# Performance work log

Hardware: AMD Instinct MI355X
Metric: run time of the kernel (lower is better)

## Reference

```python
import jax, jax.numpy as jnp
import numpy as np

# --- Cone-beam geometry (TIGRE-style defaults) ---
B, C, A, V, U = 1, 8, 120, 128, 128   # batch, channels, angles, det_rows, det_cols
NZ, NY, NX = 96, 96, 96               # volume voxels (Z, Y, X)
DSO = 1000.0                          # source-to-origin distance (mm)
DSD = 1500.0                          # source-to-detector distance (mm)
DU = DV = 1.0                         # detector pixel size (mm)
DVOX = 0.8                            # voxel size (mm)


def setup_inputs() -> dict:
    key = jax.random.key(0)
    sinogram = jax.random.normal(key, (B, C, A, V, U), dtype=jnp.float32)
    angles = jnp.arange(A, dtype=jnp.float32) * jnp.float32(2.0 * np.pi / A)
    return {"sinogram": sinogram, "angles": angles}


def _voxel_grids():
    # Centered physical coordinates of the voxel grid (mm).
    z = (jnp.arange(NZ, dtype=jnp.float32) - (NZ - 1) / 2.0) * DVOX  # [NZ]
    y = (jnp.arange(NY, dtype=jnp.float32) - (NY - 1) / 2.0) * DVOX  # [NY]
    x = (jnp.arange(NX, dtype=jnp.float32) - (NX - 1) / 2.0) * DVOX  # [NX]
    return z[:, None, None], y[None, :, None], x[None, None, :]


def _backproject(sino_bc, angles):
    """Voxel-driven cone-beam backprojection (unfiltered, matched Atb style).

    sino_bc: [BC, A, V, U] -> volume [BC, NZ, NY, NX]
    """
    BC = sino_bc.shape[0]
    zg, yg, xg = _voxel_grids()
    nvox = NZ * NY * NX

    def step(acc, inp):
        ang, s_a = inp  # s_a: [BC, V, U]
        c, s = jnp.cos(ang), jnp.sin(ang)
        # Rotate voxel coords into the source frame for this angle.
        xr = xg * c + yg * s          # [1, NY, NX] distance along source axis
        yr = -xg * s + yg * c         # [1, NY, NX] lateral coordinate
        dist = DSO - xr               # source-to-voxel-plane distance
        mag = DSD / dist              # cone-beam magnification [1, NY, NX]
        iu = jnp.broadcast_to(yr * mag / DU + (U - 1) / 2.0, (NZ, NY, NX)).reshape(nvox)
        iv = (zg * mag / DV + (V - 1) / 2.0).reshape(nvox)
        w = jnp.broadcast_to(mag * mag, (NZ, NY, NX)).reshape(nvox)  # distance weight

        valid = (iu >= 0) & (iu <= U - 1) & (iv >= 0) & (iv <= V - 1)
        u0f = jnp.floor(iu); v0f = jnp.floor(iv)
        fu = iu - u0f; fv = iv - v0f
        u0 = jnp.clip(u0f.astype(jnp.int32), 0, U - 1)
        u1 = jnp.clip(u0 + 1, 0, U - 1)
        v0 = jnp.clip(v0f.astype(jnp.int32), 0, V - 1)
        v1 = jnp.clip(v0 + 1, 0, V - 1)

        # Bilinear detector interpolation for all channels at once: [BC, nvox]
        val = (s_a[:, v0, u0] * ((1 - fv) * (1 - fu))
               + s_a[:, v0, u1] * ((1 - fv) * fu)
               + s_a[:, v1, u0] * (fv * (1 - fu))
               + s_a[:, v1, u1] * (fv * fu))
        contrib = val * (w * valid.astype(jnp.float32))
        return acc + contrib, None

    acc0 = jnp.zeros((BC, nvox), dtype=jnp.float32)
    sino_a_first = jnp.moveaxis(sino_bc, 1, 0)  # [A, BC, V, U]
    acc, _ = jax.lax.scan(step, acc0, (angles, sino_a_first))
    return acc.reshape(BC, NZ, NY, NX)


def reference(sinogram, angles):
    b, c = sinogram.shape[:2]
    vol = _backproject(sinogram.reshape(b * c, A, V, U), angles)
    return vol.reshape(b, c, NZ, NY, NX)
```

## Files before the change

kernel.cpp:

```cpp
#include <hip/hip_runtime.h>
#include <hip/hip_fp16.h>


#define A_N   120
#define V_N   128
#define U_N   128
#define NZv   96
#define NYv   96
#define NXv   96
#define C_N   8
#define ZPT   2

constexpr float DSO  = 1000.0f;
constexpr float DSD  = 1500.0f;
constexpr float DVOX = 0.8f;

#define NVOX   (NZv * NYv * NXv)
#define SINO_N (A_N * V_N * U_N)
#define CHUNK  12

struct alignas(16) H8 { __half2 h[4]; };

__global__ __launch_bounds__(256) void sino_to_h(
    const float* __restrict__ in, H8* __restrict__ out) {
  int idx = blockIdx.x * 256 + threadIdx.x;
  H8 o;
#pragma unroll
  for (int i = 0; i < 4; ++i) {
    float lo = in[(size_t)(2 * i)     * SINO_N + idx];
    float hi = in[(size_t)(2 * i + 1) * SINO_N + idx];
    o.h[i] = __floats2half2_rn(lo, hi);
  }
  out[idx] = o;
}

__global__ __launch_bounds__(256) void backproject_t8(
    const H8* __restrict__ sino,
    const float* __restrict__ angles,
    float* __restrict__ out) {
  __shared__ float s_c[A_N];
  __shared__ float s_s[A_N];
  int tid = threadIdx.x;
  if (tid < A_N) {
    float a = angles[tid];
    s_c[tid] = cosf(a);
    s_s[tid] = sinf(a);
  }
  __syncthreads();

  int lid = tid & 63;
  int wv  = tid >> 6;
  int lx  = lid & 7;
  int ly  = lid >> 3;
  int x   = blockIdx.x * 16 + (wv & 1) * 8 + lx;
  int y   = blockIdx.y * 16 + (wv >> 1) * 8 + ly;
  int z0  = blockIdx.z * ZPT;

  float xf = ((float)x - (NXv - 1) * 0.5f) * DVOX;
  float yf = ((float)y - (NYv - 1) * 0.5f) * DVOX;
  float zf[ZPT];
#pragma unroll
  for (int k = 0; k < ZPT; ++k)
    zf[k] = ((float)(z0 + k) - (NZv - 1) * 0.5f) * DVOX;

  float2  accf[ZPT][4];
  __half2 acch[ZPT][4];
#pragma unroll
  for (int k = 0; k < ZPT; ++k)
#pragma unroll
    for (int i = 0; i < 4; ++i) {
      accf[k][i] = make_float2(0.0f, 0.0f);
      acch[k][i] = __float2half2_rn(0.0f);
    }

  for (int chnk = 0; chnk < A_N / CHUNK; ++chnk) {
#pragma unroll 2
    for (int j = 0; j < CHUNK; ++j) {
      int a = chnk * CHUNK + j;
      float cs = s_c[a], sn = s_s[a];
      float xr  = xf * cs + yf * sn;
      float yr  = yf * cs - xf * sn;
      float mag = DSD * __builtin_amdgcn_rcpf(DSO - xr);
      float w   = mag * mag;

      float iu  = yr * mag + (U_N - 1) * 0.5f;
      bool uok  = (iu >= 0.0f) && (iu <= (float)(U_N - 1));
      float iuc = fminf(fmaxf(iu, 0.0f), (float)(U_N - 1));
      float u0f = fminf(floorf(iuc), (float)(U_N - 2));
      float fu  = iuc - u0f;
      float gu  = 1.0f - fu;
      int u0    = (int)u0f;
      float wu  = uok ? w : 0.0f;
      const H8* arow = sino + (size_t)(a * (V_N * U_N) + u0);

#pragma unroll
      for (int k = 0; k < ZPT; ++k) {
        float iv  = fmaf(zf[k], mag, (V_N - 1) * 0.5f);
        bool ok   = (iv >= 0.0f) && (iv <= (float)(V_N - 1));
        float ivc = fminf(fmaxf(iv, 0.0f), (float)(V_N - 1));
        float v0f = fminf(floorf(ivc), (float)(V_N - 2));
        float fv  = ivc - v0f;
        int v0    = (int)v0f;
        float wz  = ok ? wu : 0.0f;
        float wv0 = wz * (1.0f - fv);
        float wv1 = wz * fv;

        __half2 h00 = __float2half2_rn(wv0 * gu);
        __half2 h01 = __float2half2_rn(wv0 * fu);
        __half2 h10 = __float2half2_rn(wv1 * gu);
        __half2 h11 = __float2half2_rn(wv1 * fu);

        const H8* p = arow + v0 * U_N;
        H8 c00 = p[0];
        H8 c01 = p[1];
        H8 c10 = p[U_N];
        H8 c11 = p[U_N + 1];

#pragma unroll
        for (int i = 0; i < 4; ++i) {
          acch[k][i] = __hfma2(c00.h[i], h00,
                       __hfma2(c01.h[i], h01,
                       __hfma2(c10.h[i], h10,
                       __hfma2(c11.h[i], h11, acch[k][i]))));
        }
      }
    }
#pragma unroll
    for (int k = 0; k < ZPT; ++k)
#pragma unroll
      for (int i = 0; i < 4; ++i) {
        float2 sf = __half22float2(acch[k][i]);
        accf[k][i].x += sf.x;
        accf[k][i].y += sf.y;
        acch[k][i] = __float2half2_rn(0.0f);
      }
  }

#pragma unroll
  for (int k = 0; k < ZPT; ++k) {
    int vi = ((z0 + k) * NYv + y) * NXv + x;
#pragma unroll
    for (int i = 0; i < 4; ++i) {
      out[(size_t)(2 * i)     * NVOX + vi] = accf[k][i].x;
      out[(size_t)(2 * i + 1) * NVOX + vi] = accf[k][i].y;
    }
  }
}

__global__ __launch_bounds__(256) void backproject_direct(
    const float* __restrict__ sino,
    const float* __restrict__ angles,
    float* __restrict__ out) {
  __shared__ float s_c[A_N];
  __shared__ float s_s[A_N];
  int tid = threadIdx.x;
  if (tid < A_N) {
    float a = angles[tid];
    s_c[tid] = cosf(a);
    s_s[tid] = sinf(a);
  }
  __syncthreads();

  int vi = blockIdx.x * 256 + tid;
  int x = vi % NXv;
  int t = vi / NXv;
  int y = t % NYv;
  int z = t / NYv;

  float xf = ((float)x - (NXv - 1) * 0.5f) * DVOX;
  float yf = ((float)y - (NYv - 1) * 0.5f) * DVOX;
  float zf = ((float)z - (NZv - 1) * 0.5f) * DVOX;

  float acc[C_N];
#pragma unroll
  for (int c = 0; c < C_N; ++c) acc[c] = 0.0f;

  for (int a = 0; a < A_N; ++a) {
    float cs = s_c[a], sn = s_s[a];
    float xr = xf * cs + yf * sn;
    float yr = yf * cs - xf * sn;
    float mag = DSD / (DSO - xr);
    float iu = yr * mag + (U_N - 1) * 0.5f;
    float iv = zf * mag + (V_N - 1) * 0.5f;
    if (iu < 0.0f || iu > (float)(U_N - 1) || iv < 0.0f || iv > (float)(V_N - 1))
      continue;
    float u0f = floorf(iu), v0f = floorf(iv);
    float fu = iu - u0f, fv = iv - v0f;
    int u0 = (int)u0f, v0 = (int)v0f;
    int u1 = min(u0 + 1, U_N - 1);
    int v1 = min(v0 + 1, V_N - 1);
    float w = mag * mag;
    float w00 = w * (1.0f - fv) * (1.0f - fu);
    float w01 = w * (1.0f - fv) * fu;
    float w10 = w * fv * (1.0f - fu);
    float w11 = w * fv * fu;

    int b00 = (a * V_N + v0) * U_N + u0;
    int b01 = (a * V_N + v0) * U_N + u1;
    int b10 = (a * V_N + v1) * U_N + u0;
    int b11 = (a * V_N + v1) * U_N + u1;
#pragma unroll
    for (int c = 0; c < C_N; ++c) {
      const float* pc = sino + (size_t)c * SINO_N;
      acc[c] += w00 * pc[b00] + w01 * pc[b01] + w10 * pc[b10] + w11 * pc[b11];
    }
  }

#pragma unroll
  for (int c = 0; c < C_N; ++c)
    out[(size_t)c * NVOX + vi] = acc[c];
}

extern "C" void kernel_launch(void* const* d_in, const int* in_sizes, int n_in,
                              void* d_out, int out_size, void* d_ws, size_t ws_size,
                              hipStream_t stream) {
  const float* sino   = (const float*)d_in[0];
  const float* angles = (const float*)d_in[1];
  float* out = (float*)d_out;

  size_t need = (size_t)SINO_N * sizeof(H8);
  if (ws_size >= need) {
    H8* sino_h = (H8*)d_ws;
    sino_to_h<<<SINO_N / 256, 256, 0, stream>>>(sino, sino_h);
    dim3 grid(NXv / 16, NYv / 16, NZv / ZPT);
    backproject_t8<<<grid, 256, 0, stream>>>(sino_h, angles, out);
  } else {
    backproject_direct<<<NVOX / 256, 256, 0, stream>>>(sino, angles, out);
  }
}
```

Measured before the change: 219.6 us.

## Stage per-angle detector footprint in LDS with double-buffered prefetch

For each block and angle, the kernel first computes a conservative 32x6 detector bounding box covering the block's 16x16x2 voxels. Each angle's patch of packed half-precision sinogram is loaded cooperatively into a double-buffered shared-memory array, and the next angle's patch is prefetched while the current one is used. Bilinear taps then read shared memory instead of doing scattered global gathers. In exchange it adds a block-wide barrier per angle and drops the inner-loop unroll. Samples that fall outside the fixed box are clamped, so correctness depends on the box always covering the true footprint.

```diff
diff --git a/kernel.cpp b/kernel.cpp
--- a/kernel.cpp
+++ b/kernel.cpp
@@ -10,6 +10,9 @@
 #define NXv   96
 #define C_N   8
 #define ZPT   2
+#define USPAN 32
+#define VSPAN 6
+#define NREC  (USPAN * VSPAN)
 
 constexpr float DSO  = 1000.0f;
 constexpr float DSD  = 1500.0f;
@@ -34,34 +37,63 @@
   out[idx] = o;
 }
 
-__global__ __launch_bounds__(256) void backproject_t8(
+__global__ __launch_bounds__(256) void backproject_lds(
     const H8* __restrict__ sino,
     const float* __restrict__ angles,
     float* __restrict__ out) {
   __shared__ float s_c[A_N];
   __shared__ float s_s[A_N];
+  __shared__ int2  s_box[A_N];
+  __shared__ H8    s_buf[2][NREC];
+
   int tid = threadIdx.x;
+  int bx0 = blockIdx.x * 16, by0 = blockIdx.y * 16;
+  int z0  = blockIdx.z * ZPT;
+  float zf0 = ((float)z0 - (NZv - 1) * 0.5f) * DVOX;
+  float zf1 = zf0 + DVOX;
+
   if (tid < A_N) {
-    float a = angles[tid];
-    s_c[tid] = cosf(a);
-    s_s[tid] = sinf(a);
+    float ang = angles[tid];
+    float cs = cosf(ang), sn = sinf(ang);
+    s_c[tid] = cs; s_s[tid] = sn;
+    float xl = ((float)bx0        - (NXv - 1) * 0.5f) * DVOX;
+    float xh = ((float)(bx0 + 15) - (NXv - 1) * 0.5f) * DVOX;
+    float yl = ((float)by0        - (NYv - 1) * 0.5f) * DVOX;
+    float yh = ((float)(by0 + 15) - (NYv - 1) * 0.5f) * DVOX;
+    float xrA = xl*cs + yl*sn, yrA = yl*cs - xl*sn;
+    float xrB = xl*cs + yh*sn, yrB = yh*cs - xl*sn;
+    float xrC = xh*cs + yl*sn, yrC = yl*cs - xh*sn;
+    float xrD = xh*cs + yh*sn, yrD = yh*cs - xh*sn;
+    float mA = DSD * __builtin_amdgcn_rcpf(DSO - xrA);
+    float mB = DSD * __builtin_amdgcn_rcpf(DSO - xrB);
+    float mC = DSD * __builtin_amdgcn_rcpf(DSO - xrC);
+    float mD = DSD * __builtin_amdgcn_rcpf(DSO - xrD);
+    float umin = fminf(fminf(yrA*mA, yrB*mB), fminf(yrC*mC, yrD*mD))
+               + (U_N - 1) * 0.5f;
+    float mmin = fminf(fminf(mA, mB), fminf(mC, mD));
+    float mmax = fmaxf(fmaxf(mA, mB), fmaxf(mC, mD));
+    float vmin = fminf(fminf(zf0*mmin, zf0*mmax), fminf(zf1*mmin, zf1*mmax))
+               + (V_N - 1) * 0.5f;
+    int ulo = min(max((int)floorf(umin) - 1, 0), U_N - USPAN);
+    int vlo = min(max((int)floorf(vmin) - 1, 0), V_N - VSPAN);
+    s_box[tid] = make_int2(ulo, vlo);
   }
   __syncthreads();
 
-  int lid = tid & 63;
-  int wv  = tid >> 6;
-  int lx  = lid & 7;
-  int ly  = lid >> 3;
-  int x   = blockIdx.x * 16 + (wv & 1) * 8 + lx;
-  int y   = blockIdx.y * 16 + (wv >> 1) * 8 + ly;
-  int z0  = blockIdx.z * ZPT;
-
+  int lid = tid & 63, wv = tid >> 6;
+  int x = bx0 + (wv & 1) * 8 + (lid & 7);
+  int y = by0 + (wv >> 1) * 8 + (lid >> 3);
   float xf = ((float)x - (NXv - 1) * 0.5f) * DVOX;
   float yf = ((float)y - (NYv - 1) * 0.5f) * DVOX;
-  float zf[ZPT];
-#pragma unroll
-  for (int k = 0; k < ZPT; ++k)
-    zf[k] = ((float)(z0 + k) - (NZv - 1) * 0.5f) * DVOX;
+  float zf[ZPT] = { zf0, zf1 };
+
+  int sr = tid >> 5, scol = tid & 31;
+
+  if (tid < NREC) {
+    int2 b0 = s_box[0];
+    s_buf[0][tid] = sino[(size_t)((b0.y + sr) * U_N) + b0.x + scol];
+  }
+  __syncthreads();
 
   float2  accf[ZPT][4];
   __half2 acch[ZPT][4];
@@ -74,15 +106,22 @@
     }
 
   for (int chnk = 0; chnk < A_N / CHUNK; ++chnk) {
-#pragma unroll 2
     for (int j = 0; j < CHUNK; ++j) {
       int a = chnk * CHUNK + j;
+      bool more = (a + 1 < A_N);
+
+      H8 nxt;
+      if (more && tid < NREC) {
+        int2 bn = s_box[a + 1];
+        nxt = sino[(size_t)(((a + 1) * V_N + bn.y + sr) * U_N) + bn.x + scol];
+      }
+
+      int2 bc = s_box[a];
       float cs = s_c[a], sn = s_s[a];
       float xr  = xf * cs + yf * sn;
       float yr  = yf * cs - xf * sn;
       float mag = DSD * __builtin_amdgcn_rcpf(DSO - xr);
       float w   = mag * mag;
-
       float iu  = yr * mag + (U_N - 1) * 0.5f;
       bool uok  = (iu >= 0.0f) && (iu <= (float)(U_N - 1));
       float iuc = fminf(fmaxf(iu, 0.0f), (float)(U_N - 1));
@@ -91,7 +130,8 @@
       float gu  = 1.0f - fu;
       int u0    = (int)u0f;
       float wu  = uok ? w : 0.0f;
-      const H8* arow = sino + (size_t)(a * (V_N * U_N) + u0);
+      int ur    = min(max(u0 - bc.x, 0), USPAN - 2);
+      const H8* bufc = s_buf[a & 1];
 
 #pragma unroll
       for (int k = 0; k < ZPT; ++k) {
@@ -110,11 +150,12 @@
         __half2 h10 = __float2half2_rn(wv1 * gu);
         __half2 h11 = __float2half2_rn(wv1 * fu);
 
-        const H8* p = arow + v0 * U_N;
+        int vr = min(max(v0 - bc.y, 0), VSPAN - 2);
+        const H8* p = bufc + vr * USPAN + ur;
         H8 c00 = p[0];
         H8 c01 = p[1];
-        H8 c10 = p[U_N];
-        H8 c11 = p[U_N + 1];
+        H8 c10 = p[USPAN];
+        H8 c11 = p[USPAN + 1];
 
 #pragma unroll
         for (int i = 0; i < 4; ++i) {
@@ -124,6 +165,9 @@
                        __hfma2(c11.h[i], h11, acch[k][i]))));
         }
       }
+
+      if (more && tid < NREC) s_buf[(a + 1) & 1][tid] = nxt;
+      __syncthreads();
     }
 #pragma unroll
     for (int k = 0; k < ZPT; ++k)
@@ -223,7 +267,7 @@
     H8* sino_h = (H8*)d_ws;
     sino_to_h<<<SINO_N / 256, 256, 0, stream>>>(sino, sino_h);
     dim3 grid(NXv / 16, NYv / 16, NZv / ZPT);
-    backproject_t8<<<grid, 256, 0, stream>>>(sino_h, angles, out);
+    backproject_lds<<<grid, 256, 0, stream>>>(sino_h, angles, out);
   } else {
     backproject_direct<<<NVOX / 256, 256, 0, stream>>>(sino, angles, out);
   }
```

After: 255.4 us. 1.16x slower.
